# Optimization experiments

Hardware: AMD Instinct MI355X
Metric: run time of the kernel (lower is better)

Reference implementation:

```python
import jax, jax.numpy as jnp
import numpy as np

B, L, N = 32, 4096, 256
FFT_K = 5
MAX_FREQ_LEVELS = 4
LAGS = [1, 3, 6, 12, 24]


def setup_inputs() -> dict:
    key = jax.random.key(0)
    k0, k1, k2, k3, k4 = jax.random.split(key, 5)
    x = jax.random.normal(k0, (B, L, N), dtype=jnp.float32)
    # depth_gate: Linear(2->8), GELU, Linear(8->1)  (stored as x @ W + b)
    dg_w1 = jax.random.normal(k1, (2, 8), dtype=jnp.float32) * 0.5
    dg_b1 = jax.random.normal(k2, (8,), dtype=jnp.float32) * 0.1
    dg_w2 = jax.random.normal(k3, (8, 1), dtype=jnp.float32) * 0.3
    dg_b2 = jax.random.normal(k4, (1,), dtype=jnp.float32) * 0.1
    return {"x": x, "dg_w1": dg_w1, "dg_b1": dg_b1, "dg_w2": dg_w2, "dg_b2": dg_b2}


def reference(x, dg_w1, dg_b1, dg_w2, dg_b2):
    eps = 1e-8
    # ---- moment statistics (over time dim=1), torch.std is unbiased (ddof=1) ----
    mean = x.mean(axis=1, keepdims=True)                     # (B,1,N)
    std = jnp.std(x, axis=1, ddof=1, keepdims=True)          # (B,1,N)
    std_e = std + eps
    diff = x - mean
    skew = (diff ** 3).mean(axis=1, keepdims=True) / (std_e ** 3 + eps)
    kurt = (diff ** 4).mean(axis=1, keepdims=True) / (std_e ** 4 + eps) - 3.0

    # ---- FFT features with iterative multi-level top-k extraction ----
    amp = jnp.abs(jnp.fft.rfft(x, axis=1))                   # (B,F,N)
    F_bins = amp.shape[1]
    freqs = jnp.arange(F_bins, dtype=jnp.float32) / L        # (F,)
    amp_T = jnp.transpose(amp, (0, 2, 1))                    # (B,N,F)

    residual = amp_T
    aggregated = jnp.zeros_like(amp_T)
    total_energy = amp_T.mean(axis=-1, keepdims=True) + eps
    running = jnp.ones((B, N, 1), dtype=x.dtype)
    bidx = jnp.arange(B)[:, None, None]
    nidx = jnp.arange(N)[None, :, None]
    for level in range(MAX_FREQ_LEVELS):
        k_level = min(max(1, int(round(FFT_K / 2 ** level))), F_bins)
        level_amp, level_idx = jax.lax.top_k(residual, k_level)
        level_map = jnp.zeros_like(residual).at[bidx, nidx, level_idx].set(level_amp)
        residual_ratio = residual.mean(axis=-1, keepdims=True) / total_energy
        level_ratio = jnp.full_like(residual_ratio, float(level + 1) / MAX_FREQ_LEVELS)
        gate_in = jnp.concatenate([residual_ratio, level_ratio], axis=-1)    # (B,N,2)
        h = jax.nn.gelu(gate_in @ dg_w1 + dg_b1, approximate=False)
        need_deeper = jax.nn.sigmoid(h @ dg_w2 + dg_b2)                      # (B,N,1)
        aggregated = aggregated + running * level_map
        residual = residual - level_map
        running = running * need_deeper

    # hard top-k decode
    top_amp, top_idx = jax.lax.top_k(aggregated, FFT_K)      # (B,N,k)
    top_freqs = freqs[top_idx]                               # (B,N,k)
    max_amp = amp_T.max(axis=-1, keepdims=True) + eps
    top_amp_norm = top_amp / (max_amp + eps)
    fft_feat = jnp.concatenate([top_freqs, top_amp_norm], axis=-1)   # (B,N,2k)
    fft_feat = jnp.transpose(fft_feat, (0, 2, 1))                    # (B,2k,N)

    # ---- autocorrelation at fixed lags ----
    x_norm = diff / std_e
    ac = jnp.stack(
        [(x_norm[:, :-lag, :] * x_norm[:, lag:, :]).mean(axis=1) for lag in LAGS],
        axis=1,
    )  # (B, n_lags, N)

    feats = jnp.concatenate([mean, std, skew, kurt, fft_feat, ac], axis=1)  # (B,19,N)
    return jnp.transpose(feats, (0, 2, 1))  # (B,N,19)
```

## Files before the change

kernel.cpp:

```cpp
#include <hip/hip_runtime.h>
#include <math.h>

#define B_    32
#define L_    4096
#define N_    256
#define NC    2048
#define NSEG  32
#define SEGLEN (L_ / NSEG)
#define CHUNK 32
#define NCH   (SEGLEN / CHUNK)
#define NQ    9
#define NCAND 8

__device__ __forceinline__ int PD(int i) { return i + (i >> 3); }

__global__ __launch_bounds__(256, 4) void k_stats_trans(const float* __restrict__ x,
                                                        float* __restrict__ P,
                                                        float* __restrict__ xt,
                                                        int do_t) {
  __shared__ float tile[CHUNK][N_ + 1];
  const int s = blockIdx.x;
  const int b = blockIdx.y;
  const int n = threadIdx.x;
  const int l0 = s * SEGLEN;
  const float* xp = x + (size_t)b * L_ * N_ + n;
  float* xtb = xt + (size_t)b * N_ * L_;

  float prev[CHUNK];
#pragma unroll
  for (int j = 0; j < CHUNK; ++j) {
    const int l = l0 - CHUNK + j;
    prev[j] = (l >= 0) ? xp[(size_t)l * N_] : 0.0f;
  }
  float s1 = 0.f, s2 = 0.f, s3 = 0.f, s4 = 0.f;
  float c1 = 0.f, c3 = 0.f, c6 = 0.f, c12 = 0.f, c24 = 0.f;
  for (int c = 0; c < NCH; ++c) {
    const int lb = l0 + c * CHUNK;
    float cur[CHUNK];
#pragma unroll
    for (int j = 0; j < CHUNK; ++j) cur[j] = xp[(size_t)(lb + j) * N_];
#pragma unroll
    for (int j = 0; j < CHUNK; ++j) {
      const float v = cur[j], v2 = v * v;
      s1 += v; s2 += v2; s3 += v2 * v; s4 += v2 * v2;
    }
#pragma unroll
    for (int j = 0; j < CHUNK; ++j) {
      const float v = cur[j];
      c1  += v * ((j >= 1)  ? cur[j - 1]  : prev[CHUNK + j - 1]);
      c3  += v * ((j >= 3)  ? cur[j - 3]  : prev[CHUNK + j - 3]);
      c6  += v * ((j >= 6)  ? cur[j - 6]  : prev[CHUNK + j - 6]);
      c12 += v * ((j >= 12) ? cur[j - 12] : prev[CHUNK + j - 12]);
      c24 += v * ((j >= 24) ? cur[j - 24] : prev[CHUNK + j - 24]);
    }
    if (do_t) {
#pragma unroll
      for (int j = 0; j < CHUNK; ++j) tile[j][n] = cur[j];
      __syncthreads();
#pragma unroll
      for (int it = 0; it < 8; ++it) {
        const int g  = n + 256 * it;
        const int np = g >> 3;
        const int j4 = g & 7;
        float4 w;
        w.x = tile[4 * j4 + 0][np];
        w.y = tile[4 * j4 + 1][np];
        w.z = tile[4 * j4 + 2][np];
        w.w = tile[4 * j4 + 3][np];
        *(float4*)(xtb + (size_t)np * L_ + lb + 4 * j4) = w;
      }
      __syncthreads();
    }
#pragma unroll
    for (int j = 0; j < CHUNK; ++j) prev[j] = cur[j];
  }
  float* Pp = P + (size_t)(s * B_ + b) * NQ * N_ + n;
  Pp[0 * N_] = s1; Pp[1 * N_] = s2; Pp[2 * N_] = s3; Pp[3 * N_] = s4;
  Pp[4 * N_] = c1; Pp[5 * N_] = c3; Pp[6 * N_] = c6; Pp[7 * N_] = c12; Pp[8 * N_] = c24;
}

__global__ __launch_bounds__(256) void k_stats_final(const float* __restrict__ x,
                                                     const float* __restrict__ P,
                                                     float* __restrict__ out) {
  const int b = blockIdx.x;
  const int n = threadIdx.x;
  float S[NQ];
#pragma unroll
  for (int q = 0; q < NQ; ++q) S[q] = 0.0f;
  for (int s = 0; s < NSEG; ++s) {
    const float* Pp = P + (size_t)(s * B_ + b) * NQ * N_ + n;
#pragma unroll
    for (int q = 0; q < NQ; ++q) S[q] += Pp[q * N_];
  }
  const float Lf = (float)L_;
  const float mu = S[0] / Lf;
  float ssd = S[1] - Lf * mu * mu;
  ssd = fmaxf(ssd, 0.0f);
  const float stdv = sqrtf(ssd / (Lf - 1.0f));
  const float se  = stdv + 1e-8f;
  const float m3 = (S[2] - 3.0f * mu * S[1] + 2.0f * Lf * mu * mu * mu) / Lf;
  const float m4 = (S[3] - 4.0f * mu * S[2] + 6.0f * mu * mu * S[1]
                    - 3.0f * Lf * mu * mu * mu * mu) / Lf;
  const float se2 = se * se;
  const float skew = m3 / (se2 * se + 1e-8f);
  const float kurt = m4 / (se2 * se2 + 1e-8f) - 3.0f;

  const float* xp = x + (size_t)b * L_ * N_ + n;
  float hl[5], tl[5];
  {
    float hs = 0.0f, ts = 0.0f;
#pragma unroll
    for (int t = 0; t < 24; ++t) {
      hs += xp[(size_t)t * N_];
      ts += xp[(size_t)(L_ - 1 - t) * N_];
      if (t == 0)  { hl[0] = hs; tl[0] = ts; }
      if (t == 2)  { hl[1] = hs; tl[1] = ts; }
      if (t == 5)  { hl[2] = hs; tl[2] = ts; }
      if (t == 11) { hl[3] = hs; tl[3] = ts; }
      if (t == 23) { hl[4] = hs; tl[4] = ts; }
    }
  }
  float* op = out + ((size_t)b * N_ + n) * 19;
  op[0] = mu; op[1] = stdv; op[2] = skew; op[3] = kurt;
  const int lags[5] = {1, 3, 6, 12, 24};
  const float inv_se2 = 1.0f / se2;
#pragma unroll
  for (int i = 0; i < 5; ++i) {
    const float cnt = (float)(L_ - lags[i]);
    const float SA = S[0] - tl[i];
    const float SB = S[0] - hl[i];
    const float num = S[4 + i] - mu * (SA + SB) + cnt * mu * mu;
    op[14 + i] = num * inv_se2 / cnt;
  }
}

__device__ __forceinline__ void dft8(float (&vr)[8], float (&vi)[8]) {
  const float C7 = 0.70710678118654752f;
  float t0r = vr[0] + vr[4], t0i = vi[0] + vi[4];
  float t1r = vr[0] - vr[4], t1i = vi[0] - vi[4];
  float t2r = vr[2] + vr[6], t2i = vi[2] + vi[6];
  float t3r = vr[2] - vr[6], t3i = vi[2] - vi[6];
  float E0r = t0r + t2r, E0i = t0i + t2i;
  float E2r = t0r - t2r, E2i = t0i - t2i;
  float E1r = t1r + t3i, E1i = t1i - t3r;
  float E3r = t1r - t3i, E3i = t1i + t3r;
  float u0r = vr[1] + vr[5], u0i = vi[1] + vi[5];
  float u1r = vr[1] - vr[5], u1i = vi[1] - vi[5];
  float u2r = vr[3] + vr[7], u2i = vi[3] + vi[7];
  float u3r = vr[3] - vr[7], u3i = vi[3] - vi[7];
  float O0r = u0r + u2r, O0i = u0i + u2i;
  float O2r = u0r - u2r, O2i = u0i - u2i;
  float O1r = u1r + u3i, O1i = u1i - u3r;
  float O3r = u1r - u3i, O3i = u1i + u3r;
  vr[0] = E0r + O0r; vi[0] = E0i + O0i;
  vr[4] = E0r - O0r; vi[4] = E0i - O0i;
  float a1r = C7 * (O1r + O1i), a1i = C7 * (O1i - O1r);
  vr[1] = E1r + a1r; vi[1] = E1i + a1i;
  vr[5] = E1r - a1r; vi[5] = E1i - a1i;
  vr[2] = E2r + O2i; vi[2] = E2i - O2r;
  vr[6] = E2r - O2i; vi[6] = E2i + O2r;
  float a3r = C7 * (O3i - O3r), a3i = -C7 * (O3r + O3i);
  vr[3] = E3r + a3r; vi[3] = E3i + a3i;
  vr[7] = E3r - a3r; vi[7] = E3i - a3i;
}

__device__ __forceinline__ void twid8(float (&vr)[8], float (&vi)[8], float w1r, float w1i) {
  float w2r = w1r * w1r - w1i * w1i, w2i = 2.f * w1r * w1i;
  float w3r = w2r * w1r - w2i * w1i, w3i = w2r * w1i + w2i * w1r;
  float w4r = w2r * w2r - w2i * w2i, w4i = 2.f * w2r * w2i;
  float w5r = w3r * w2r - w3i * w2i, w5i = w3r * w2i + w3i * w2r;
  float w6r = w3r * w3r - w3i * w3i, w6i = 2.f * w3r * w3i;
  float w7r = w4r * w3r - w4i * w3i, w7i = w4r * w3i + w4i * w3r;
  float t;
  t = vr[1] * w1r - vi[1] * w1i; vi[1] = vr[1] * w1i + vi[1] * w1r; vr[1] = t;
  t = vr[2] * w2r - vi[2] * w2i; vi[2] = vr[2] * w2i + vi[2] * w2r; vr[2] = t;
  t = vr[3] * w3r - vi[3] * w3i; vi[3] = vr[3] * w3i + vi[3] * w3r; vr[3] = t;
  t = vr[4] * w4r - vi[4] * w4i; vi[4] = vr[4] * w4i + vi[4] * w4r; vr[4] = t;
  t = vr[5] * w5r - vi[5] * w5i; vi[5] = vr[5] * w5i + vi[5] * w5r; vr[5] = t;
  t = vr[6] * w6r - vi[6] * w6i; vi[6] = vr[6] * w6i + vi[6] * w6r; vr[6] = t;
  t = vr[7] * w7r - vi[7] * w7i; vi[7] = vr[7] * w7i + vi[7] * w7r; vr[7] = t;
}

__global__ __launch_bounds__(256, 6) void k_fft_top(const float* __restrict__ base, int stride,
                                                    float* __restrict__ out) {
  __shared__ float XR[2304];
  __shared__ float XI[2304];
  __shared__ float TWR[256];
  __shared__ float TWI[256];
  __shared__ float RVb[2][4];
  __shared__ int   RIb[2][4];
  __shared__ double DA[NCAND];
  const int tid = threadIdx.x;
  const int bn  = blockIdx.x;

  const float ang = -3.14159265358979323846f * (float)tid * (1.0f / 2048.0f);
  const float s4 = __sinf(ang), c4 = __cosf(ang);
  const float tb4r = c4, tb4i = s4;
  const float cn = c4 * c4 - s4 * s4;
  const float sn = 2.0f * c4 * s4;
  TWR[tid] = cn; TWI[tid] = sn;

  float vr[8], vi[8];
  if (stride == 1) {
    const float2* src2 = (const float2*)(base + (size_t)bn * L_);
#pragma unroll
    for (int r = 0; r < 8; ++r) {
      const float2 v = src2[tid + 256 * r];
      vr[r] = v.x; vi[r] = v.y;
    }
  } else {
    const float* src = base + (size_t)(bn >> 8) * ((size_t)L_ * N_) + (bn & (N_ - 1));
#pragma unroll
    for (int r = 0; r < 8; ++r) {
      vr[r] = src[(size_t)(2 * (tid + 256 * r)) * N_];
      vi[r] = src[(size_t)(2 * (tid + 256 * r) + 1) * N_];
    }
  }

  dft8(vr, vi);
  twid8(vr, vi, cn, sn);
#pragma unroll
  for (int m = 0; m < 8; ++m) {
    XR[PD(8 * tid + m)] = vr[m];
    XI[PD(8 * tid + m)] = vi[m];
  }
  __syncthreads();

#pragma unroll
  for (int st = 0; st < 2; ++st) {
    const int s = (st == 0) ? 8 : 64;
#pragma unroll
    for (int r = 0; r < 8; ++r) {
      vr[r] = XR[PD(tid + 256 * r)];
      vi[r] = XI[PD(tid + 256 * r)];
    }
    __syncthreads();
    const int tb = tid & ~(s - 1);
    dft8(vr, vi);
    twid8(vr, vi, TWR[tb], TWI[tb]);
    const int wb = tid + 7 * tb;
#pragma unroll
    for (int m = 0; m < 8; ++m) {
      XR[PD(wb + m * s)] = vr[m];
      XI[PD(wb + m * s)] = vi[m];
    }
    __syncthreads();
  }

  {
    float ar[8], ai[8];
#pragma unroll
    for (int h = 0; h < 2; ++h) {
      const int i = tid + 256 * h;
#pragma unroll
      for (int r = 0; r < 4; ++r) {
        ar[4 * h + r] = XR[PD(i + 512 * r)];
        ai[4 * h + r] = XI[PD(i + 512 * r)];
      }
    }
    __syncthreads();
#pragma unroll
    for (int h = 0; h < 2; ++h) {
      const int i = tid + 256 * h;
      const float x0r = ar[4*h+0], x0i = ai[4*h+0], x1r = ar[4*h+1], x1i = ai[4*h+1];
      const float x2r = ar[4*h+2], x2i = ai[4*h+2], x3r = ar[4*h+3], x3i = ai[4*h+3];
      const float t0r = x0r + x2r, t0i = x0i + x2i;
      const float t1r = x0r - x2r, t1i = x0i - x2i;
      const float t2r = x1r + x3r, t2i = x1i + x3i;
      const float t3r = x1r - x3r, t3i = x1i - x3i;
      XR[PD(i)]        = t0r + t2r;  XI[PD(i)]        = t0i + t2i;
      XR[PD(i + 512)]  = t1r + t3i;  XI[PD(i + 512)]  = t1i - t3r;
      XR[PD(i + 1024)] = t0r - t2r;  XI[PD(i + 1024)] = t0i - t2i;
      XR[PD(i + 1536)] = t1r - t3i;  XI[PD(i + 1536)] = t1i + t3r;
    }
    __syncthreads();
  }

  const float WAC[4] = {1.f, 0.92387953f, 0.70710678f, 0.38268343f};
  const float WAS[4] = {0.f, 0.38268343f, 0.70710678f, 0.92387953f};
  float av[4], am[4];
#pragma unroll
  for (int j = 0; j < 4; ++j) {
    const int k  = tid + 256 * j;
    const int kr = (2048 - k) & 2047;
    const float zar = XR[PD(k)],  zai = XI[PD(k)];
    const float zbr = XR[PD(kr)], zbi = -XI[PD(kr)];
    const float Er = 0.5f * (zar + zbr), Ei = 0.5f * (zai + zbi);
    const float Or = 0.5f * (zai - zbi), Oi = -0.5f * (zar - zbr);
    const float cv = WAC[j] * tb4r + WAS[j] * tb4i;
    const float sv = WAC[j] * tb4i - WAS[j] * tb4r;
    const float pr = cv * Or - sv * Oi, pi = cv * Oi + sv * Or;
    const float Xr = Er + pr, Xi = Ei + pi;
    const float Mr = Er - pr, Mi = Ei - pi;
    av[j] = sqrtf(Xr * Xr + Xi * Xi);
    am[j] = sqrtf(Mr * Mr + Mi * Mi);
  }
  float a1024 = -1.f;
  if (tid == 0) {
    const float zr = XR[PD(1024)], zi = XI[PD(1024)];
    a1024 = sqrtf(zr * zr + zi * zi);
  }

  const int lane = tid & 63, wid = tid >> 6;
  float bv = -1.f; int bi = 1 << 30;
#pragma unroll
  for (int j = 0; j < 4; ++j) {
    const int k = tid + 256 * j;
    if (av[j] > bv || (av[j] == bv && k < bi)) { bv = av[j]; bi = k; }
    const int mk = 2048 - k;
    if (am[j] > bv || (am[j] == bv && mk < bi)) { bv = am[j]; bi = mk; }
  }
  if (tid == 0 && a1024 > bv) { bv = a1024; bi = 1024; }

  float tv[NCAND]; int ti[NCAND];
#pragma unroll
  for (int rr = 0; rr < NCAND; ++rr) {
    float rv = bv; int ri = bi;
#pragma unroll
    for (int off = 32; off > 0; off >>= 1) {
      const float v2 = __shfl_down(rv, off);
      const int   i2 = __shfl_down(ri, off);
      if (v2 > rv || (v2 == rv && i2 < ri)) { rv = v2; ri = i2; }
    }
    if (lane == 0) { RVb[rr & 1][wid] = rv; RIb[rr & 1][wid] = ri; }
    __syncthreads();
    float mv = RVb[rr & 1][0]; int mi = RIb[rr & 1][0];
#pragma unroll
    for (int w = 1; w < 4; ++w) {
      const float v2 = RVb[rr & 1][w]; const int i2 = RIb[rr & 1][w];
      if (v2 > mv || (v2 == mv && i2 < mi)) { mv = v2; mi = i2; }
    }
    tv[rr] = mv; ti[rr] = mi;
#pragma unroll
    for (int j = 0; j < 4; ++j) {
      if (tid + 256 * j == mi) av[j] = -2.f;
      if (2048 - tid - 256 * j == mi) am[j] = -2.f;
    }
    if (tid == 0 && mi == 1024) a1024 = -2.f;
    bv = -1.f; bi = 1 << 30;
#pragma unroll
    for (int j = 0; j < 4; ++j) {
      const int k = tid + 256 * j;
      if (av[j] > bv || (av[j] == bv && k < bi)) { bv = av[j]; bi = k; }
      const int mk = 2048 - k;
      if (am[j] > bv || (am[j] == bv && mk < bi)) { bv = am[j]; bi = mk; }
    }
    if (tid == 0 && a1024 > bv) { bv = a1024; bi = 1024; }
  }

  int need = 0;
  {
    const float thr = 1e-3f * tv[0];
#pragma unroll
    for (int r = 0; r < 5; ++r) {
      if (tv[r] - tv[r + 1] < thr) need = 1;
    }
  }

  if (need) {
    const int g = tid >> 5;
    const int j = tid & 31;
    int k = ti[0];
#pragma unroll
    for (int r = 1; r < NCAND; ++r) { if (g == r) k = ti[r]; }
    const int t0 = 128 * j;
    const int e0 = (int)(((long long)k * (long long)t0) & 4095LL);
    double sp, cp;  sincos(-2.0 * 3.14159265358979323846 * (double)e0 / 4096.0, &sp, &cp);
    double sw, cw;  sincos(-2.0 * 3.14159265358979323846 * (double)k  / 4096.0, &sw, &cw);
    double ar = 0.0, ai = 0.0;
    if (stride == 1) {
      const float* xr_ = base + (size_t)bn * L_ + t0;
      for (int t = 0; t < 128; ++t) {
        const double xv = (double)xr_[t];
        ar += xv * cp; ai += xv * sp;
        const double ncp = cp * cw - sp * sw;
        sp = cp * sw + sp * cw; cp = ncp;
      }
    } else {
      const float* xr_ = base + (size_t)(bn >> 8) * ((size_t)L_ * N_) + (bn & (N_ - 1));
      for (int t = 0; t < 128; ++t) {
        const double xv = (double)xr_[(size_t)(t0 + t) * N_];
        ar += xv * cp; ai += xv * sp;
        const double ncp = cp * cw - sp * sw;
        sp = cp * sw + sp * cw; cp = ncp;
      }
    }
#pragma unroll
    for (int off = 16; off > 0; off >>= 1) {
      ar += __shfl_down(ar, off, 32);
      ai += __shfl_down(ai, off, 32);
    }
    if (j == 0) DA[g] = sqrt(ar * ar + ai * ai);
    __syncthreads();
    if (tid == 0) {
      double da[NCAND]; int di[NCAND];
#pragma unroll
      for (int r = 0; r < NCAND; ++r) { da[r] = DA[r]; di[r] = ti[r]; }
      for (int i2 = 1; i2 < NCAND; ++i2) {
        const double v = da[i2]; const int ii = di[i2];
        int p = i2 - 1;
        while (p >= 0 && (da[p] < v || (da[p] == v && di[p] > ii))) {
          da[p + 1] = da[p]; di[p + 1] = di[p]; --p;
        }
        da[p + 1] = v; di[p + 1] = ii;
      }
      float* op = out + (size_t)bn * 19;
      const double den = da[0] + 2e-8;
#pragma unroll
      for (int r = 0; r < 5; ++r) {
        op[4 + r] = (float)di[r] * (1.0f / (float)L_);
        op[9 + r] = (float)(da[r] / den);
      }
    }
  } else if (tid == 0) {
    float* op = out + (size_t)bn * 19;
    const float den = tv[0] + 2e-8f;
#pragma unroll
    for (int r = 0; r < 5; ++r) {
      op[4 + r] = (float)ti[r] * (1.0f / (float)L_);
      op[9 + r] = tv[r] / den;
    }
  }
}

extern "C" void kernel_launch(void* const* d_in, const int* in_sizes, int n_in,
                              void* d_out, int out_size, void* d_ws, size_t ws_size,
                              hipStream_t stream) {
  const float* x = (const float*)d_in[0];
  float* out = (float*)d_out;
  float* ws  = (float*)d_ws;

  const size_t xt_elems   = (size_t)B_ * N_ * L_;
  const size_t part_elems = (size_t)NSEG * B_ * NQ * N_;
  const bool use_xt = ws_size >= (xt_elems + part_elems) * sizeof(float);
  float* xt = ws;
  float* P  = use_xt ? (ws + xt_elems) : ws;

  k_stats_trans<<<dim3(NSEG, B_), 256, 0, stream>>>(x, P, use_xt ? xt : nullptr,
                                                    use_xt ? 1 : 0);
  k_stats_final<<<B_, 256, 0, stream>>>(x, P, out);
  if (use_xt) {
    k_fft_top<<<B_ * N_, 256, 0, stream>>>(xt, 1, out);
  } else {
    k_fft_top<<<B_ * N_, 256, 0, stream>>>(x, N_, out);
  }
}
```

Measured before the change: 365.5 us.

## Interleave FFT shared buffers as float2, defer sqrt, and rescan only owner thread

Stores the FFT working arrays and twiddles as interleaved float2 in shared memory so each complex element is moved with one 64-bit access. The top-k candidate search now ranks squared magnitudes and takes sqrt only for the eight selected values. After each selection round only the thread owning the removed bin recomputes its local best instead of all threads. The launch-bounds occupancy hint drops from 6 to 4, which gives the compiler more registers per thread but allows fewer resident blocks.

```diff
diff --git a/kernel.cpp b/kernel.cpp
--- a/kernel.cpp
+++ b/kernel.cpp
@@ -181,12 +181,10 @@
   t = vr[7] * w7r - vi[7] * w7i; vi[7] = vr[7] * w7i + vi[7] * w7r; vr[7] = t;
 }
 
-__global__ __launch_bounds__(256, 6) void k_fft_top(const float* __restrict__ base, int stride,
+__global__ __launch_bounds__(256, 4) void k_fft_top(const float* __restrict__ base, int stride,
                                                     float* __restrict__ out) {
-  __shared__ float XR[2304];
-  __shared__ float XI[2304];
-  __shared__ float TWR[256];
-  __shared__ float TWI[256];
+  __shared__ float2 X[2304];
+  __shared__ float2 TW[256];
   __shared__ float RVb[2][4];
   __shared__ int   RIb[2][4];
   __shared__ double DA[NCAND];
@@ -198,7 +196,7 @@
   const float tb4r = c4, tb4i = s4;
   const float cn = c4 * c4 - s4 * s4;
   const float sn = 2.0f * c4 * s4;
-  TWR[tid] = cn; TWI[tid] = sn;
+  TW[tid] = make_float2(cn, sn);
 
   float vr[8], vi[8];
   if (stride == 1) {
@@ -220,10 +218,7 @@
   dft8(vr, vi);
   twid8(vr, vi, cn, sn);
 #pragma unroll
-  for (int m = 0; m < 8; ++m) {
-    XR[PD(8 * tid + m)] = vr[m];
-    XI[PD(8 * tid + m)] = vi[m];
-  }
+  for (int m = 0; m < 8; ++m) X[PD(8 * tid + m)] = make_float2(vr[m], vi[m]);
   __syncthreads();
 
 #pragma unroll
@@ -231,47 +226,42 @@
     const int s = (st == 0) ? 8 : 64;
 #pragma unroll
     for (int r = 0; r < 8; ++r) {
-      vr[r] = XR[PD(tid + 256 * r)];
-      vi[r] = XI[PD(tid + 256 * r)];
+      const float2 z = X[PD(tid + 256 * r)];
+      vr[r] = z.x; vi[r] = z.y;
     }
     __syncthreads();
     const int tb = tid & ~(s - 1);
     dft8(vr, vi);
-    twid8(vr, vi, TWR[tb], TWI[tb]);
+    const float2 w = TW[tb];
+    twid8(vr, vi, w.x, w.y);
     const int wb = tid + 7 * tb;
 #pragma unroll
-    for (int m = 0; m < 8; ++m) {
-      XR[PD(wb + m * s)] = vr[m];
-      XI[PD(wb + m * s)] = vi[m];
-    }
+    for (int m = 0; m < 8; ++m) X[PD(wb + m * s)] = make_float2(vr[m], vi[m]);
     __syncthreads();
   }
 
   {
-    float ar[8], ai[8];
+    float2 a[8];
 #pragma unroll
     for (int h = 0; h < 2; ++h) {
       const int i = tid + 256 * h;
 #pragma unroll
-      for (int r = 0; r < 4; ++r) {
-        ar[4 * h + r] = XR[PD(i + 512 * r)];
-        ai[4 * h + r] = XI[PD(i + 512 * r)];
-      }
+      for (int r = 0; r < 4; ++r) a[4 * h + r] = X[PD(i + 512 * r)];
     }
     __syncthreads();
 #pragma unroll
     for (int h = 0; h < 2; ++h) {
       const int i = tid + 256 * h;
-      const float x0r = ar[4*h+0], x0i = ai[4*h+0], x1r = ar[4*h+1], x1i = ai[4*h+1];
-      const float x2r = ar[4*h+2], x2i = ai[4*h+2], x3r = ar[4*h+3], x3i = ai[4*h+3];
+      const float x0r = a[4*h+0].x, x0i = a[4*h+0].y, x1r = a[4*h+1].x, x1i = a[4*h+1].y;
+      const float x2r = a[4*h+2].x, x2i = a[4*h+2].y, x3r = a[4*h+3].x, x3i = a[4*h+3].y;
       const float t0r = x0r + x2r, t0i = x0i + x2i;
       const float t1r = x0r - x2r, t1i = x0i - x2i;
       const float t2r = x1r + x3r, t2i = x1i + x3i;
       const float t3r = x1r - x3r, t3i = x1i - x3i;
-      XR[PD(i)]        = t0r + t2r;  XI[PD(i)]        = t0i + t2i;
-      XR[PD(i + 512)]  = t1r + t3i;  XI[PD(i + 512)]  = t1i - t3r;
-      XR[PD(i + 1024)] = t0r - t2r;  XI[PD(i + 1024)] = t0i - t2i;
-      XR[PD(i + 1536)] = t1r - t3i;  XI[PD(i + 1536)] = t1i + t3r;
+      X[PD(i)]        = make_float2(t0r + t2r, t0i + t2i);
+      X[PD(i + 512)]  = make_float2(t1r + t3i, t1i - t3r);
+      X[PD(i + 1024)] = make_float2(t0r - t2r, t0i - t2i);
+      X[PD(i + 1536)] = make_float2(t1r - t3i, t1i + t3r);
     }
     __syncthreads();
   }
@@ -283,22 +273,22 @@
   for (int j = 0; j < 4; ++j) {
     const int k  = tid + 256 * j;
     const int kr = (2048 - k) & 2047;
-    const float zar = XR[PD(k)],  zai = XI[PD(k)];
-    const float zbr = XR[PD(kr)], zbi = -XI[PD(kr)];
-    const float Er = 0.5f * (zar + zbr), Ei = 0.5f * (zai + zbi);
-    const float Or = 0.5f * (zai - zbi), Oi = -0.5f * (zar - zbr);
+    const float2 za = X[PD(k)];
+    const float2 zb = X[PD(kr)];
+    const float Er = 0.5f * (za.x + zb.x), Ei = 0.5f * (za.y - zb.y);
+    const float Or = 0.5f * (za.y + zb.y), Oi = 0.5f * (zb.x - za.x);
     const float cv = WAC[j] * tb4r + WAS[j] * tb4i;
     const float sv = WAC[j] * tb4i - WAS[j] * tb4r;
     const float pr = cv * Or - sv * Oi, pi = cv * Oi + sv * Or;
     const float Xr = Er + pr, Xi = Ei + pi;
     const float Mr = Er - pr, Mi = Ei - pi;
-    av[j] = sqrtf(Xr * Xr + Xi * Xi);
-    am[j] = sqrtf(Mr * Mr + Mi * Mi);
+    av[j] = Xr * Xr + Xi * Xi;
+    am[j] = Mr * Mr + Mi * Mi;
   }
   float a1024 = -1.f;
   if (tid == 0) {
-    const float zr = XR[PD(1024)], zi = XI[PD(1024)];
-    a1024 = sqrtf(zr * zr + zi * zi);
+    const float2 z = X[PD(1024)];
+    a1024 = z.x * z.x + z.y * z.y;
   }
 
   const int lane = tid & 63, wid = tid >> 6;
@@ -331,29 +321,38 @@
       if (v2 > mv || (v2 == mv && i2 < mi)) { mv = v2; mi = i2; }
     }
     tv[rr] = mv; ti[rr] = mi;
-#pragma unroll
-    for (int j = 0; j < 4; ++j) {
-      if (tid + 256 * j == mi) av[j] = -2.f;
-      if (2048 - tid - 256 * j == mi) am[j] = -2.f;
-    }
-    if (tid == 0 && mi == 1024) a1024 = -2.f;
-    bv = -1.f; bi = 1 << 30;
-#pragma unroll
-    for (int j = 0; j < 4; ++j) {
-      const int k = tid + 256 * j;
-      if (av[j] > bv || (av[j] == bv && k < bi)) { bv = av[j]; bi = k; }
-      const int mk = 2048 - k;
-      if (am[j] > bv || (am[j] == bv && mk < bi)) { bv = am[j]; bi = mk; }
-    }
-    if (tid == 0 && a1024 > bv) { bv = a1024; bi = 1024; }
-  }
-
+    bool own = false;
+    if (mi == 1024) {
+      if (tid == 0) { a1024 = -1.f; own = true; }
+    } else {
+      const int d = (mi < 1024) ? mi : (2048 - mi);
+      if ((d & 255) == tid) {
+        own = true;
+        if (mi < 1024) av[d >> 8] = -1.f; else am[d >> 8] = -1.f;
+      }
+    }
+    if (own) {
+      bv = -1.f; bi = 1 << 30;
+#pragma unroll
+      for (int j = 0; j < 4; ++j) {
+        const int k = tid + 256 * j;
+        if (av[j] > bv || (av[j] == bv && k < bi)) { bv = av[j]; bi = k; }
+        const int mk = 2048 - k;
+        if (am[j] > bv || (am[j] == bv && mk < bi)) { bv = am[j]; bi = mk; }
+      }
+      if (tid == 0 && a1024 > bv) { bv = a1024; bi = 1024; }
+    }
+  }
+
+  float ta[NCAND];
+#pragma unroll
+  for (int r = 0; r < NCAND; ++r) ta[r] = sqrtf(tv[r]);
   int need = 0;
   {
-    const float thr = 1e-3f * tv[0];
+    const float thr = 1e-3f * ta[0];
 #pragma unroll
     for (int r = 0; r < 5; ++r) {
-      if (tv[r] - tv[r + 1] < thr) need = 1;
+      if (ta[r] - ta[r + 1] < thr) need = 1;
     }
   }
 
@@ -414,11 +413,11 @@
     }
   } else if (tid == 0) {
     float* op = out + (size_t)bn * 19;
-    const float den = tv[0] + 2e-8f;
+    const float den = ta[0] + 2e-8f;
 #pragma unroll
     for (int r = 0; r < 5; ++r) {
       op[4 + r] = (float)ti[r] * (1.0f / (float)L_);
-      op[9 + r] = tv[r] / den;
+      op[9 + r] = ta[r] / den;
     }
   }
 }
```

Result: slower. 422.9 us (+15.7%).

## Reassign rfft bins contiguously, shuffle twiddles, and rescan only the owning thread in top-k

Applied to the files above, without the earlier changes.

Twiddle factors for the radix-8 stages now come from a wavefront shuffle of per-lane registers, so the shared-memory twiddle tables and their stores go away. The rfft post-processing now has each thread compute 8 contiguous-stride bins k=tid+256j, plus the Nyquist bin 2048 from XR[0]-XI[0], instead of paired k/2048-k bins. This removes the mirrored branch and simplifies tie-breaking. In the iterative top-k, only the thread owning the selected bin marks it dead with a bitmask and recomputes its local max, which avoids a full per-thread rescan every round. The launch-bounds occupancy hint drops from 6 to 4, and tie-break ordering within a thread changes slightly.

```diff
diff --git a/kernel.cpp b/kernel.cpp
--- a/kernel.cpp
+++ b/kernel.cpp
@@ -181,12 +181,10 @@
   t = vr[7] * w7r - vi[7] * w7i; vi[7] = vr[7] * w7i + vi[7] * w7r; vr[7] = t;
 }
 
-__global__ __launch_bounds__(256, 6) void k_fft_top(const float* __restrict__ base, int stride,
+__global__ __launch_bounds__(256, 4) void k_fft_top(const float* __restrict__ base, int stride,
                                                     float* __restrict__ out) {
   __shared__ float XR[2304];
   __shared__ float XI[2304];
-  __shared__ float TWR[256];
-  __shared__ float TWI[256];
   __shared__ float RVb[2][4];
   __shared__ int   RIb[2][4];
   __shared__ double DA[NCAND];
@@ -198,7 +196,6 @@
   const float tb4r = c4, tb4i = s4;
   const float cn = c4 * c4 - s4 * s4;
   const float sn = 2.0f * c4 * s4;
-  TWR[tid] = cn; TWI[tid] = sn;
 
   float vr[8], vi[8];
   if (stride == 1) {
@@ -236,8 +233,10 @@
     }
     __syncthreads();
     const int tb = tid & ~(s - 1);
+    const float wr = __shfl(cn, tb & 63);
+    const float wi = __shfl(sn, tb & 63);
     dft8(vr, vi);
-    twid8(vr, vi, TWR[tb], TWI[tb]);
+    twid8(vr, vi, wr, wi);
     const int wb = tid + 7 * tb;
 #pragma unroll
     for (int m = 0; m < 8; ++m) {
@@ -276,11 +275,13 @@
     __syncthreads();
   }
 
-  const float WAC[4] = {1.f, 0.92387953f, 0.70710678f, 0.38268343f};
-  const float WAS[4] = {0.f, 0.38268343f, 0.70710678f, 0.92387953f};
-  float av[4], am[4];
-#pragma unroll
-  for (int j = 0; j < 4; ++j) {
+  const float WAC[9] = {1.f, 0.92387953f, 0.70710678f, 0.38268343f, 0.f,
+                        -0.38268343f, -0.70710678f, -0.92387953f, -1.f};
+  const float WAS[9] = {0.f, 0.38268343f, 0.70710678f, 0.92387953f, 1.f,
+                        0.92387953f, 0.70710678f, 0.38268343f, 0.f};
+  float av[8];
+#pragma unroll
+  for (int j = 0; j < 8; ++j) {
     const int k  = tid + 256 * j;
     const int kr = (2048 - k) & 2047;
     const float zar = XR[PD(k)],  zai = XI[PD(k)];
@@ -289,28 +290,22 @@
     const float Or = 0.5f * (zai - zbi), Oi = -0.5f * (zar - zbr);
     const float cv = WAC[j] * tb4r + WAS[j] * tb4i;
     const float sv = WAC[j] * tb4i - WAS[j] * tb4r;
-    const float pr = cv * Or - sv * Oi, pi = cv * Oi + sv * Or;
-    const float Xr = Er + pr, Xi = Ei + pi;
-    const float Mr = Er - pr, Mi = Ei - pi;
+    const float Xr = Er + cv * Or - sv * Oi;
+    const float Xi = Ei + cv * Oi + sv * Or;
     av[j] = sqrtf(Xr * Xr + Xi * Xi);
-    am[j] = sqrtf(Mr * Mr + Mi * Mi);
-  }
-  float a1024 = -1.f;
-  if (tid == 0) {
-    const float zr = XR[PD(1024)], zi = XI[PD(1024)];
-    a1024 = sqrtf(zr * zr + zi * zi);
-  }
+  }
+  float a2048 = -1.f;
+  if (tid == 0) a2048 = fabsf(XR[0] - XI[0]);
 
   const int lane = tid & 63, wid = tid >> 6;
+  int dead = 0;
   float bv = -1.f; int bi = 1 << 30;
 #pragma unroll
-  for (int j = 0; j < 4; ++j) {
+  for (int j = 0; j < 8; ++j) {
     const int k = tid + 256 * j;
-    if (av[j] > bv || (av[j] == bv && k < bi)) { bv = av[j]; bi = k; }
-    const int mk = 2048 - k;
-    if (am[j] > bv || (am[j] == bv && mk < bi)) { bv = am[j]; bi = mk; }
-  }
-  if (tid == 0 && a1024 > bv) { bv = a1024; bi = 1024; }
+    if (av[j] > bv) { bv = av[j]; bi = k; }
+  }
+  if (tid == 0 && a2048 > bv) { bv = a2048; bi = 2048; }
 
   float tv[NCAND]; int ti[NCAND];
 #pragma unroll
@@ -331,21 +326,17 @@
       if (v2 > mv || (v2 == mv && i2 < mi)) { mv = v2; mi = i2; }
     }
     tv[rr] = mv; ti[rr] = mi;
-#pragma unroll
-    for (int j = 0; j < 4; ++j) {
-      if (tid + 256 * j == mi) av[j] = -2.f;
-      if (2048 - tid - 256 * j == mi) am[j] = -2.f;
-    }
-    if (tid == 0 && mi == 1024) a1024 = -2.f;
-    bv = -1.f; bi = 1 << 30;
-#pragma unroll
-    for (int j = 0; j < 4; ++j) {
-      const int k = tid + 256 * j;
-      if (av[j] > bv || (av[j] == bv && k < bi)) { bv = av[j]; bi = k; }
-      const int mk = 2048 - k;
-      if (am[j] > bv || (am[j] == bv && mk < bi)) { bv = am[j]; bi = mk; }
-    }
-    if (tid == 0 && a1024 > bv) { bv = a1024; bi = 1024; }
+    const bool own = (mi == 2048) ? (tid == 0) : ((mi & 255) == tid);
+    if (own) {
+      dead |= 1 << ((mi == 2048) ? 8 : (mi >> 8));
+      bv = -1.f; bi = 1 << 30;
+#pragma unroll
+      for (int j = 0; j < 8; ++j) {
+        const int k = tid + 256 * j;
+        if (!(dead & (1 << j)) && av[j] > bv) { bv = av[j]; bi = k; }
+      }
+      if (tid == 0 && !(dead & 256) && a2048 > bv) { bv = a2048; bi = 2048; }
+    }
   }
 
   int need = 0;
```

Result: slower. 373.5 us (+2.2%).
